# Kernel optimization log

Hardware: AMD Instinct MI355X
Metric: run time of the kernel (lower is better)

Reference implementation:

```python
import jax, jax.numpy as jnp
import numpy as np

N_HEADS = 16


def setup_inputs() -> dict:
    key = jax.random.key(0)
    ks = jax.random.split(key, 6)
    B, S, E = 2, 2048, 1024
    scale = 1.0 / np.sqrt(E)
    return {
        "X": jax.random.normal(ks[0], (B, S, E), dtype=jnp.float32),
        "Wq": jax.random.normal(ks[1], (E, E), dtype=jnp.float32) * scale,
        "Wk": jax.random.normal(ks[2], (E, E), dtype=jnp.float32) * scale,
        "Wv": jax.random.normal(ks[3], (E, E), dtype=jnp.float32) * scale,
        "Wp": jax.random.normal(ks[4], (E, E), dtype=jnp.float32) * scale,
        "bp": jnp.zeros((E,), dtype=jnp.float32),
    }


def reference(X, Wq, Wk, Wv, Wp, bp):
    B, S, E = X.shape
    H = N_HEADS
    dk = E // H
    # qkv projections (Linear with weight [out,in] -> x @ W.T), split heads
    q = (X @ Wq.T).reshape(B, S, H, dk).transpose(0, 2, 1, 3)  # [B,H,S,dk]
    k = (X @ Wk.T).reshape(B, S, H, dk).transpose(0, 2, 1, 3)
    v = (X @ Wv.T).reshape(B, S, H, dk).transpose(0, 2, 1, 3)
    scores = jnp.einsum('bhqd,bhkd->bhqk', q, k) / jnp.sqrt(jnp.asarray(dk, X.dtype))
    causal = jnp.tril(jnp.ones((S, S), dtype=bool))  # [S,S]
    scores = jnp.where(causal[None, None], scores, jnp.asarray(-jnp.inf, X.dtype))
    attn = jax.nn.softmax(scores, axis=-1)  # [B,H,S,S]
    y = jnp.einsum('bhqk,bhkd->bhqd', attn, v)  # [B,H,S,dk]
    y = y.transpose(0, 2, 1, 3).reshape(B, S, E)
    return y @ Wp.T + bp
```

## Files before the change

kernel.cpp:

```cpp
#include <hip/hip_runtime.h>

typedef unsigned short u16;
typedef __bf16 bf16x8 __attribute__((ext_vector_type(8)));
typedef float f32x4 __attribute__((ext_vector_type(4)));
typedef unsigned short u16x8 __attribute__((ext_vector_type(8)));
typedef unsigned short u16x4 __attribute__((ext_vector_type(4)));

union B8 { u16x8 u; bf16x8 b; };

#define MFMA_BF16(a, b, c) __builtin_amdgcn_mfma_f32_16x16x32_bf16((a), (b), (c), 0, 0, 0)

__device__ __forceinline__ u16 f2bf(float f) {
  unsigned x = __float_as_uint(f);
  unsigned r = x + 0x7fffu + ((x >> 16) & 1u);
  return (u16)(r >> 16);
}

__device__ __forceinline__ unsigned cvt_pk_bf16(float lo, float hi) {
  unsigned r;
  asm("v_cvt_pk_bf16_f32 %0, %1, %2" : "=v"(r) : "v"(lo), "v"(hi));
  return r;
}

__device__ __forceinline__ void gl2lds16(const void* g, void* l) {
  __builtin_amdgcn_global_load_lds(
      (const __attribute__((address_space(1))) void*)g,
      (__attribute__((address_space(3))) void*)l, 16, 0, 0);
}

__global__ __launch_bounds__(256) void cast5_kernel(
    const float* __restrict__ X, const float* __restrict__ Wq,
    const float* __restrict__ Wk, const float* __restrict__ Wv,
    const float* __restrict__ Wp, u16* __restrict__ Xb, u16* __restrict__ Wqb,
    u16* __restrict__ Wkb, u16* __restrict__ Wvb, u16* __restrict__ Wpb) {
  size_t i = ((size_t)blockIdx.x * 256 + threadIdx.x) * 4;
  const float* src;
  u16* dst;
  size_t off;
  if (i < 4194304) {
    src = X; dst = Xb; off = i;
  } else if (i < 5242880) {
    src = Wq; dst = Wqb; off = i - 4194304;
  } else if (i < 6291456) {
    src = Wk; dst = Wkb; off = i - 5242880;
  } else if (i < 7340032) {
    src = Wv; dst = Wvb; off = i - 6291456;
  } else {
    src = Wp; dst = Wpb; off = i - 7340032;
  }
  float4 v = *(const float4*)(src + off);
  u16x4 o;
  o[0] = f2bf(v.x); o[1] = f2bf(v.y); o[2] = f2bf(v.z); o[3] = f2bf(v.w);
  *(u16x4*)(dst + off) = o;
}

__device__ __forceinline__ void gemm_body(const u16* __restrict__ A,
                                          const u16* __restrict__ Bw,
                                          void* __restrict__ Cout,
                                          const float* __restrict__ bias,
                                          int bm, int bn, int mode, u16* Asm,
                                          u16* Bsm) {
  const int Kd = 1024, N = 1024;
  int tid = threadIdx.x;
  int lane = tid & 63, w = tid >> 6;
  int wr = w >> 1, wc = w & 1;
  int l16 = lane & 15, lg = lane >> 4;

  const u16* Abase = A + (size_t)bm * 128 * Kd;
  const u16* Bbase = Bw + (size_t)bn * 128 * Kd;

  f32x4 acc[4][4] = {};

  for (int kt = 0; kt < Kd / 64; ++kt) {
    int k0 = kt * 64;
#pragma unroll
    for (int i = 0; i < 4; ++i) {
      int uu = i * 256 + tid;
      int r = uu >> 3;
      int s = (uu & 7) ^ (r & 7);
      gl2lds16(Abase + (size_t)r * Kd + k0 + s * 8, Asm + i * 2048 + w * 512);
      gl2lds16(Bbase + (size_t)r * Kd + k0 + s * 8, Bsm + i * 2048 + w * 512);
    }
    asm volatile("s_waitcnt vmcnt(0)" ::: "memory");
    __syncthreads();

    B8 af[4][2], bfr[4][2];
#pragma unroll
    for (int mi = 0; mi < 4; ++mi)
#pragma unroll
      for (int kk = 0; kk < 2; ++kk) {
        int r = wr * 64 + mi * 16 + l16;
        int s = kk * 4 + lg;
        af[mi][kk].u = *(const u16x8*)((const char*)Asm + r * 128 + ((s ^ (r & 7)) << 4));
      }
#pragma unroll
    for (int ni = 0; ni < 4; ++ni)
#pragma unroll
      for (int kk = 0; kk < 2; ++kk) {
        int r = wc * 64 + ni * 16 + l16;
        int s = kk * 4 + lg;
        bfr[ni][kk].u = *(const u16x8*)((const char*)Bsm + r * 128 + ((s ^ (r & 7)) << 4));
      }
#pragma unroll
    for (int mi = 0; mi < 4; ++mi)
#pragma unroll
      for (int ni = 0; ni < 4; ++ni) {
        acc[mi][ni] = MFMA_BF16(af[mi][0].b, bfr[ni][0].b, acc[mi][ni]);
        acc[mi][ni] = MFMA_BF16(af[mi][1].b, bfr[ni][1].b, acc[mi][ni]);
      }
    __syncthreads();
  }

  if (mode == 2) {
#pragma unroll
    for (int mi = 0; mi < 4; ++mi)
#pragma unroll
      for (int ni = 0; ni < 4; ++ni) {
        int col = bn * 128 + wc * 64 + ni * 16 + l16;
        int hh = col >> 6, d = col & 63;
        int row0 = bm * 128 + wr * 64 + mi * 16 + lg * 4;
        int bb = row0 >> 11, s0 = row0 & 2047;
        u16x4 pk;
#pragma unroll
        for (int j = 0; j < 4; ++j) pk[j] = f2bf(acc[mi][ni][j]);
        *(u16x4*)((u16*)Cout + ((size_t)(bb * 16 + hh) * 64 + d) * 2048 + s0) = pk;
      }
  } else if (mode == 3) {
#pragma unroll
    for (int mi = 0; mi < 4; ++mi)
#pragma unroll
      for (int ni = 0; ni < 4; ++ni) {
        int col = bn * 128 + wc * 64 + ni * 16 + l16;
#pragma unroll
        for (int j = 0; j < 4; ++j) {
          int row = bm * 128 + wr * 64 + mi * 16 + lg * 4 + j;
          ((float*)Cout)[(size_t)row * N + col] = acc[mi][ni][j] + bias[col];
        }
      }
  } else {
    float scale = (mode == 1) ? 0.18033688011112042f : 1.0f;
#pragma unroll
    for (int mi = 0; mi < 4; ++mi)
#pragma unroll
      for (int ni = 0; ni < 4; ++ni) {
        int col = bn * 128 + wc * 64 + ni * 16 + l16;
#pragma unroll
        for (int j = 0; j < 4; ++j) {
          int row = bm * 128 + wr * 64 + mi * 16 + lg * 4 + j;
          ((u16*)Cout)[(size_t)row * N + col] = f2bf(acc[mi][ni][j] * scale);
        }
      }
  }
}

__global__ __launch_bounds__(256) void gemm_qkv_kernel(
    const u16* __restrict__ Xb, const u16* __restrict__ Wqb,
    const u16* __restrict__ Wkb, const u16* __restrict__ Wvb,
    u16* __restrict__ Qb, u16* __restrict__ Kb, u16* __restrict__ Vt) {
  __shared__ __align__(16) u16 Asm[128 * 64];
  __shared__ __align__(16) u16 Bsm[128 * 64];
  const u16* Bw;
  void* C;
  int mode;
  if (blockIdx.z == 0) { Bw = Wqb; C = Qb; mode = 1; }
  else if (blockIdx.z == 1) { Bw = Wkb; C = Kb; mode = 0; }
  else { Bw = Wvb; C = Vt; mode = 2; }
  gemm_body(Xb, Bw, C, nullptr, blockIdx.y, blockIdx.x, mode, Asm, Bsm);
}

__global__ __launch_bounds__(256) void gemm_proj_kernel(
    const u16* __restrict__ Y1, const u16* __restrict__ Wpb,
    float* __restrict__ out, const float* __restrict__ bias) {
  __shared__ __align__(16) u16 Asm[128 * 64];
  __shared__ __align__(16) u16 Bsm[128 * 64];
  gemm_body(Y1, Wpb, out, bias, blockIdx.y, blockIdx.x, 3, Asm, Bsm);
}

__global__ __launch_bounds__(256, 4) void attn_kernel(const u16* __restrict__ Q,
                                                      const u16* __restrict__ K,
                                                      const u16* __restrict__ Vt,
                                                      u16* __restrict__ Y) {
  __shared__ __align__(16) u16 Kl[2][64 * 64];
  __shared__ __align__(16) u16 Vl[2][64 * 64];
  __shared__ __align__(16) u16 Pl[4][16 * 64];

  const int E = 1024, S = 2048;
  int tid = threadIdx.x;
  int lane = tid & 63, w = tid >> 6;
  int l16 = lane & 15, lg = lane >> 4;

  int bid = blockIdx.x;
  int bh = bid & 31;
  int qt = 31 - (bid >> 5);
  int b = bh >> 4, h = bh & 15;

  const u16* Qb = Q + (size_t)b * S * E + (size_t)h * 64;
  const u16* Kb = K + (size_t)b * S * E + (size_t)h * 64;
  const u16* Vb = Vt + (size_t)bh * 64 * 2048;

  auto stage = [&](int bf, int t) {
#pragma unroll
    for (int i = 0; i < 2; ++i) {
      int uu = i * 256 + tid;
      int r = uu >> 3;
      int s = (uu & 7) ^ (r & 7);
      gl2lds16(Kb + (size_t)(t * 64 + r) * E + s * 8, &Kl[bf][i * 2048 + w * 512]);
      gl2lds16(Vb + (size_t)r * 2048 + t * 64 + s * 8, &Vl[bf][i * 2048 + w * 512]);
    }
  };

  B8 qa[2];
#pragma unroll
  for (int kk = 0; kk < 2; ++kk)
    qa[kk].u = *(const u16x8*)(Qb + (size_t)(qt * 64 + w * 16 + l16) * E + kk * 32 + lg * 8);

  f32x4 o[4] = {};
  float mrun = -1e30f, lrun = 0.f;
  int qrow = w * 16 + l16;

  stage(0, 0);
  int buf = 0;
  int total = qt + 1;

  for (int t = 0; t < total; ++t) {
    asm volatile("s_waitcnt vmcnt(0)" ::: "memory");
    __syncthreads();
    if (t + 1 < total) stage(buf ^ 1, t + 1);

    f32x4 sa[4] = {};
    __builtin_amdgcn_s_setprio(1);
#pragma unroll
    for (int nb = 0; nb < 4; ++nb) {
      B8 kf0, kf1;
      int r = nb * 16 + l16;
      kf0.u = *(const u16x8*)((const char*)&Kl[buf][0] + r * 128 + ((lg ^ (r & 7)) << 4));
      kf1.u = *(const u16x8*)((const char*)&Kl[buf][0] + r * 128 + (((4 + lg) ^ (r & 7)) << 4));
      sa[nb] = MFMA_BF16(kf0.b, qa[0].b, sa[nb]);
      sa[nb] = MFMA_BF16(kf1.b, qa[1].b, sa[nb]);
    }
    __builtin_amdgcn_s_setprio(0);

    float p[16];
    bool domask = (t == qt);
    float tm = -1e30f;
#pragma unroll
    for (int nb = 0; nb < 4; ++nb)
#pragma unroll
      for (int j = 0; j < 4; ++j) {
        float sv = sa[nb][j];
        if (domask) {
          int kv = nb * 16 + lg * 4 + j;
          if (kv > qrow) sv = -1e30f;
        }
        p[nb * 4 + j] = sv;
      }
    {
      float t0[8];
#pragma unroll
      for (int i = 0; i < 8; ++i) t0[i] = fmaxf(p[i], p[i + 8]);
#pragma unroll
      for (int i = 0; i < 4; ++i) t0[i] = fmaxf(t0[i], t0[i + 4]);
      tm = fmaxf(fmaxf(t0[0], t0[1]), fmaxf(t0[2], t0[3]));
    }
    tm = fmaxf(tm, __shfl_xor(tm, 16));
    tm = fmaxf(tm, __shfl_xor(tm, 32));

    if (__any(tm > mrun)) {
      float mn = fmaxf(mrun, tm);
      float corr = __builtin_amdgcn_exp2f(mrun - mn);
      mrun = mn;
      lrun *= corr;
      float cj[4];
#pragma unroll
      for (int j = 0; j < 4; ++j)
        cj[j] = __shfl(corr, (lane & 48) | (lg * 4 + j));
#pragma unroll
      for (int nb = 0; nb < 4; ++nb)
#pragma unroll
        for (int j = 0; j < 4; ++j) o[nb][j] *= cj[j];
    }

    float rs = 0.f;
#pragma unroll
    for (int i = 0; i < 16; ++i) {
      float pe = __builtin_amdgcn_exp2f(p[i] - mrun);
      p[i] = pe;
      rs += pe;
    }
    rs += __shfl_xor(rs, 16);
    rs += __shfl_xor(rs, 32);
    lrun += rs;

#pragma unroll
    for (int nb = 0; nb < 4; ++nb) {
      unsigned w0 = cvt_pk_bf16(p[nb * 4 + 0], p[nb * 4 + 1]);
      unsigned w1 = cvt_pk_bf16(p[nb * 4 + 2], p[nb * 4 + 3]);
      union { u16x4 v; unsigned u[2]; } pk;
      pk.u[0] = w0; pk.u[1] = w1;
      int s = nb * 2 + (lg >> 1);
      *(u16x4*)((char*)&Pl[w][0] + l16 * 128 + (((s ^ (l16 & 7))) << 4) + (lg & 1) * 8) = pk.v;
    }
    asm volatile("s_waitcnt lgkmcnt(0)" ::: "memory");
    __builtin_amdgcn_sched_barrier(0);

    B8 pa[2];
#pragma unroll
    for (int kk = 0; kk < 2; ++kk)
      pa[kk].u = *(const u16x8*)((const char*)&Pl[w][0] + l16 * 128 + (((kk * 4 + lg) ^ (l16 & 7)) << 4));
    __builtin_amdgcn_s_setprio(1);
#pragma unroll
    for (int nb = 0; nb < 4; ++nb) {
      B8 vf0, vf1;
      int r = nb * 16 + l16;
      vf0.u = *(const u16x8*)((const char*)&Vl[buf][0] + r * 128 + ((lg ^ (r & 7)) << 4));
      vf1.u = *(const u16x8*)((const char*)&Vl[buf][0] + r * 128 + (((4 + lg) ^ (r & 7)) << 4));
      o[nb] = MFMA_BF16(pa[0].b, vf0.b, o[nb]);
      o[nb] = MFMA_BF16(pa[1].b, vf1.b, o[nb]);
    }
    __builtin_amdgcn_s_setprio(0);
    buf ^= 1;
  }

  float inv[4];
#pragma unroll
  for (int j = 0; j < 4; ++j) {
    float lj = __shfl(lrun, (lane & 48) | (lg * 4 + j));
    inv[j] = 1.0f / lj;
  }
#pragma unroll
  for (int nb = 0; nb < 4; ++nb)
#pragma unroll
    for (int j = 0; j < 4; ++j) {
      int row = qt * 64 + w * 16 + lg * 4 + j;
      int col = h * 64 + nb * 16 + l16;
      Y[((size_t)b * S + row) * E + col] = f2bf(o[nb][j] * inv[j]);
    }
}

extern "C" void kernel_launch(void* const* d_in, const int* in_sizes, int n_in,
                              void* d_out, int out_size, void* d_ws,
                              size_t ws_size, hipStream_t stream) {
  const float* X = (const float*)d_in[0];
  const float* Wq = (const float*)d_in[1];
  const float* Wk = (const float*)d_in[2];
  const float* Wv = (const float*)d_in[3];
  const float* Wp = (const float*)d_in[4];
  const float* bp = (const float*)d_in[5];
  float* out = (float*)d_out;

  char* ws = (char*)d_ws;
  const size_t MB = 1ull << 20;
  u16* Xb = (u16*)(ws + 0 * MB);
  u16* Wqb = (u16*)(ws + 8 * MB);
  u16* Wkb = (u16*)(ws + 10 * MB);
  u16* Wvb = (u16*)(ws + 12 * MB);
  u16* Wpb = (u16*)(ws + 14 * MB);
  u16* Qb = (u16*)(ws + 16 * MB);
  u16* Kb = (u16*)(ws + 24 * MB);
  u16* VtB = (u16*)(ws + 32 * MB);
  u16* Y1 = (u16*)(ws + 40 * MB);

  cast5_kernel<<<8192, 256, 0, stream>>>(X, Wq, Wk, Wv, Wp, Xb, Wqb, Wkb, Wvb, Wpb);
  gemm_qkv_kernel<<<dim3(8, 32, 3), 256, 0, stream>>>(Xb, Wqb, Wkb, Wvb, Qb, Kb, VtB);
  attn_kernel<<<1024, 256, 0, stream>>>(Qb, Kb, VtB, Y1);
  gemm_proj_kernel<<<dim3(8, 32), 256, 0, stream>>>(Y1, Wpb, out, bp);
}
```

Baseline: 125.2 us.

## Fuse QKV into one 256x256-tile pipelined GEMM and lazily rescale softmax

Replaces the three-way QKV GEMM (128x128 tiles, single-buffered, 256 threads) with one kernel over a concatenated 3072-wide weight. The new kernel uses 256x256 tiles, 512 threads, double-buffered direct global-to-LDS loads split into K-halves, a swizzled block order and MFMA priority hints. The epilogue routes each column range to Q (scaled), K, or transposed V. Separately, the attention kernel now rescales its online-softmax accumulators only when the running max grows by more than 8 in log2 units, skipping most correction passes. The cost is larger unnormalised exponentials, which relies on fp32/bf16 headroom. The fused GEMM also assumes the Wq/Wk/Wv bf16 copies sit contiguously in the workspace.

```diff
diff --git a/kernel.cpp b/kernel.cpp
--- a/kernel.cpp
+++ b/kernel.cpp
@@ -54,12 +54,153 @@
   *(u16x4*)(dst + off) = o;
 }
 
+template <int N0>
+__device__ __forceinline__ void mfma16(f32x4 (&acc)[8][4], B8 (&af)[8], B8& b0,
+                                       B8& b1) {
+  __builtin_amdgcn_s_setprio(1);
+#pragma unroll
+  for (int m = 0; m < 8; ++m) {
+    acc[m][N0] = MFMA_BF16(af[m].b, b0.b, acc[m][N0]);
+    acc[m][N0 + 1] = MFMA_BF16(af[m].b, b1.b, acc[m][N0 + 1]);
+  }
+  __builtin_amdgcn_s_setprio(0);
+}
+
+__global__ __launch_bounds__(512, 2) void gemm_qkv256(
+    const u16* __restrict__ Xb, const u16* __restrict__ Wb,
+    u16* __restrict__ Qb, u16* __restrict__ Kb, u16* __restrict__ Vt) {
+  __shared__ __align__(16) u16 Al[2][2][256 * 32];
+  __shared__ __align__(16) u16 Bl[2][2][256 * 32];
+
+  int tid = threadIdx.x, lane = tid & 63, w = tid >> 6;
+  int wr = w >> 2, wc = w & 3;
+  int l16 = lane & 15, lg = lane >> 4;
+
+  int bid = blockIdx.x;
+  int swz = (bid & 7) * 24 + (bid >> 3);
+  int bm = swz / 12, bn = swz % 12;
+
+  const u16* Ag = Xb + (size_t)bm * 256 * 1024;
+  const u16* Bg = Wb + (size_t)bn * 256 * 1024;
+
+  int srow = w * 16 + (lane >> 2);
+  int scol = lane & 3;
+
+  auto stA = [&](int buf, int kh, int kt) {
+#pragma unroll
+    for (int p2 = 0; p2 < 2; ++p2) {
+      int r = p2 * 128 + srow;
+      int sl = scol ^ ((r >> 1) & 3);
+      gl2lds16(Ag + (size_t)r * 1024 + kt * 64 + kh * 32 + sl * 8,
+               (char*)&Al[buf][kh][0] + (size_t)(p2 * 128 + w * 16) * 64);
+    }
+  };
+  auto stB = [&](int buf, int kh, int kt) {
+#pragma unroll
+    for (int p2 = 0; p2 < 2; ++p2) {
+      int r = p2 * 128 + srow;
+      int sl = scol ^ ((r >> 1) & 3);
+      gl2lds16(Bg + (size_t)r * 1024 + kt * 64 + kh * 32 + sl * 8,
+               (char*)&Bl[buf][kh][0] + (size_t)(p2 * 128 + w * 16) * 64);
+    }
+  };
+  auto ldA = [&](int buf, int kk, B8 (&af)[8]) {
+#pragma unroll
+    for (int m = 0; m < 8; ++m) {
+      int r = wr * 128 + m * 16 + l16;
+      af[m].u = *(const u16x8*)((const char*)&Al[buf][kk][0] + r * 64 +
+                                ((lg ^ ((r >> 1) & 3)) << 4));
+    }
+  };
+  auto ldB = [&](int buf, int kk, int nf, B8& bf) {
+    int r = wc * 64 + nf * 16 + l16;
+    bf.u = *(const u16x8*)((const char*)&Bl[buf][kk][0] + r * 64 +
+                           ((lg ^ ((r >> 1) & 3)) << 4));
+  };
+
+  f32x4 acc[8][4] = {};
+
+  stA(0, 0, 0); stB(0, 0, 0);
+  stA(0, 1, 0); stB(0, 1, 0);
+  stA(1, 0, 1); stB(1, 0, 1);
+  asm volatile("s_waitcnt vmcnt(8)" ::: "memory");
+  __builtin_amdgcn_s_barrier();
+
+  B8 af[8], b0, b1;
+  for (int I = 0; I < 8; ++I) {
+    int p = 2 * I;
+    bool last = (I == 7);
+    stA(1, 1, p + 1);
+    ldA(0, 0, af); ldB(0, 0, 0, b0); ldB(0, 0, 1, b1);
+    mfma16<0>(acc, af, b0, b1);
+    stB(1, 1, p + 1);
+    ldB(0, 0, 2, b0); ldB(0, 0, 3, b1);
+    mfma16<2>(acc, af, b0, b1);
+    if (last) asm volatile("s_waitcnt vmcnt(0)" ::: "memory");
+    else      asm volatile("s_waitcnt vmcnt(8)" ::: "memory");
+    __builtin_amdgcn_s_barrier();
+    if (!last) stA(0, 0, p + 2);
+    ldA(0, 1, af); ldB(0, 1, 0, b0); ldB(0, 1, 1, b1);
+    mfma16<0>(acc, af, b0, b1);
+    if (!last) stB(0, 0, p + 2);
+    ldB(0, 1, 2, b0); ldB(0, 1, 3, b1);
+    mfma16<2>(acc, af, b0, b1);
+    if (last) asm volatile("s_waitcnt vmcnt(0)" ::: "memory");
+    else      asm volatile("s_waitcnt vmcnt(8)" ::: "memory");
+    __builtin_amdgcn_s_barrier();
+    if (!last) stA(0, 1, p + 2);
+    ldA(1, 0, af); ldB(1, 0, 0, b0); ldB(1, 0, 1, b1);
+    mfma16<0>(acc, af, b0, b1);
+    if (!last) stB(0, 1, p + 2);
+    ldB(1, 0, 2, b0); ldB(1, 0, 3, b1);
+    mfma16<2>(acc, af, b0, b1);
+    if (last) asm volatile("s_waitcnt vmcnt(0)" ::: "memory");
+    else      asm volatile("s_waitcnt vmcnt(8)" ::: "memory");
+    __builtin_amdgcn_s_barrier();
+    if (!last) stA(1, 0, p + 3);
+    ldA(1, 1, af); ldB(1, 1, 0, b0); ldB(1, 1, 1, b1);
+    mfma16<0>(acc, af, b0, b1);
+    if (!last) stB(1, 0, p + 3);
+    ldB(1, 1, 2, b0); ldB(1, 1, 3, b1);
+    mfma16<2>(acc, af, b0, b1);
+    if (!last) {
+      asm volatile("s_waitcnt vmcnt(8)" ::: "memory");
+      __builtin_amdgcn_s_barrier();
+    }
+  }
+
+  const float QSCALE = 0.18033688011112042f;
+#pragma unroll
+  for (int m = 0; m < 8; ++m)
+#pragma unroll
+    for (int nf = 0; nf < 4; ++nf) {
+      int colg = bn * 256 + wc * 64 + nf * 16 + l16;
+      int rowg = bm * 256 + wr * 128 + m * 16 + lg * 4;
+      if (bn < 4) {
+#pragma unroll
+        for (int j = 0; j < 4; ++j)
+          Qb[(size_t)(rowg + j) * 1024 + colg] = f2bf(acc[m][nf][j] * QSCALE);
+      } else if (bn < 8) {
+#pragma unroll
+        for (int j = 0; j < 4; ++j)
+          Kb[(size_t)(rowg + j) * 1024 + (colg - 1024)] = f2bf(acc[m][nf][j]);
+      } else {
+        int cv = colg - 2048;
+        int hh = cv >> 6, d = cv & 63;
+        int bb = rowg >> 11, s0 = rowg & 2047;
+        u16x4 pk;
+#pragma unroll
+        for (int j = 0; j < 4; ++j) pk[j] = f2bf(acc[m][nf][j]);
+        *(u16x4*)(Vt + ((size_t)(bb * 16 + hh) * 64 + d) * 2048 + s0) = pk;
+      }
+    }
+}
+
 __device__ __forceinline__ void gemm_body(const u16* __restrict__ A,
                                           const u16* __restrict__ Bw,
-                                          void* __restrict__ Cout,
+                                          float* __restrict__ Cout,
                                           const float* __restrict__ bias,
-                                          int bm, int bn, int mode, u16* Asm,
-                                          u16* Bsm) {
+                                          int bm, int bn, u16* Asm, u16* Bsm) {
   const int Kd = 1024, N = 1024;
   int tid = threadIdx.x;
   int lane = tid & 63, w = tid >> 6;
@@ -111,61 +252,17 @@
     __syncthreads();
   }
 
-  if (mode == 2) {
-#pragma unroll
-    for (int mi = 0; mi < 4; ++mi)
-#pragma unroll
-      for (int ni = 0; ni < 4; ++ni) {
-        int col = bn * 128 + wc * 64 + ni * 16 + l16;
-        int hh = col >> 6, d = col & 63;
-        int row0 = bm * 128 + wr * 64 + mi * 16 + lg * 4;
-        int bb = row0 >> 11, s0 = row0 & 2047;
-        u16x4 pk;
-#pragma unroll
-        for (int j = 0; j < 4; ++j) pk[j] = f2bf(acc[mi][ni][j]);
-        *(u16x4*)((u16*)Cout + ((size_t)(bb * 16 + hh) * 64 + d) * 2048 + s0) = pk;
-      }
-  } else if (mode == 3) {
-#pragma unroll
-    for (int mi = 0; mi < 4; ++mi)
-#pragma unroll
-      for (int ni = 0; ni < 4; ++ni) {
-        int col = bn * 128 + wc * 64 + ni * 16 + l16;
-#pragma unroll
-        for (int j = 0; j < 4; ++j) {
-          int row = bm * 128 + wr * 64 + mi * 16 + lg * 4 + j;
-          ((float*)Cout)[(size_t)row * N + col] = acc[mi][ni][j] + bias[col];
-        }
-      }
-  } else {
-    float scale = (mode == 1) ? 0.18033688011112042f : 1.0f;
-#pragma unroll
-    for (int mi = 0; mi < 4; ++mi)
-#pragma unroll
-      for (int ni = 0; ni < 4; ++ni) {
-        int col = bn * 128 + wc * 64 + ni * 16 + l16;
-#pragma unroll
-        for (int j = 0; j < 4; ++j) {
-          int row = bm * 128 + wr * 64 + mi * 16 + lg * 4 + j;
-          ((u16*)Cout)[(size_t)row * N + col] = f2bf(acc[mi][ni][j] * scale);
-        }
-      }
-  }
-}
-
-__global__ __launch_bounds__(256) void gemm_qkv_kernel(
-    const u16* __restrict__ Xb, const u16* __restrict__ Wqb,
-    const u16* __restrict__ Wkb, const u16* __restrict__ Wvb,
-    u16* __restrict__ Qb, u16* __restrict__ Kb, u16* __restrict__ Vt) {
-  __shared__ __align__(16) u16 Asm[128 * 64];
-  __shared__ __align__(16) u16 Bsm[128 * 64];
-  const u16* Bw;
-  void* C;
-  int mode;
-  if (blockIdx.z == 0) { Bw = Wqb; C = Qb; mode = 1; }
-  else if (blockIdx.z == 1) { Bw = Wkb; C = Kb; mode = 0; }
-  else { Bw = Wvb; C = Vt; mode = 2; }
-  gemm_body(Xb, Bw, C, nullptr, blockIdx.y, blockIdx.x, mode, Asm, Bsm);
+#pragma unroll
+  for (int mi = 0; mi < 4; ++mi)
+#pragma unroll
+    for (int ni = 0; ni < 4; ++ni) {
+      int col = bn * 128 + wc * 64 + ni * 16 + l16;
+#pragma unroll
+      for (int j = 0; j < 4; ++j) {
+        int row = bm * 128 + wr * 64 + mi * 16 + lg * 4 + j;
+        Cout[(size_t)row * N + col] = acc[mi][ni][j] + bias[col];
+      }
+    }
 }
 
 __global__ __launch_bounds__(256) void gemm_proj_kernel(
@@ -173,7 +270,7 @@
     float* __restrict__ out, const float* __restrict__ bias) {
   __shared__ __align__(16) u16 Asm[128 * 64];
   __shared__ __align__(16) u16 Bsm[128 * 64];
-  gemm_body(Y1, Wpb, out, bias, blockIdx.y, blockIdx.x, 3, Asm, Bsm);
+  gemm_body(Y1, Wpb, out, bias, blockIdx.y, blockIdx.x, Asm, Bsm);
 }
 
 __global__ __launch_bounds__(256, 4) void attn_kernel(const u16* __restrict__ Q,
@@ -265,7 +362,7 @@
     tm = fmaxf(tm, __shfl_xor(tm, 16));
     tm = fmaxf(tm, __shfl_xor(tm, 32));
 
-    if (__any(tm > mrun)) {
+    if (__any(tm > mrun + 8.f)) {
       float mn = fmaxf(mrun, tm);
       float corr = __builtin_amdgcn_exp2f(mrun - mn);
       mrun = mn;
@@ -361,7 +458,7 @@
   u16* Y1 = (u16*)(ws + 40 * MB);
 
   cast5_kernel<<<8192, 256, 0, stream>>>(X, Wq, Wk, Wv, Wp, Xb, Wqb, Wkb, Wvb, Wpb);
-  gemm_qkv_kernel<<<dim3(8, 32, 3), 256, 0, stream>>>(Xb, Wqb, Wkb, Wvb, Qb, Kb, VtB);
+  gemm_qkv256<<<192, 512, 0, stream>>>(Xb, Wqb, Qb, Kb, VtB);
   attn_kernel<<<1024, 256, 0, stream>>>(Qb, Kb, VtB, Y1);
   gemm_proj_kernel<<<dim3(8, 32), 256, 0, stream>>>(Y1, Wpb, out, bp);
 }
```

Result: faster. 113.4 us (-9.4%).
